# Kernel tuning notes

Measured on AMD Instinct MI355X. Metric: run time of the kernel, lower is better.

Reference implementation:

```python
import jax, jax.numpy as jnp
import numpy as np

S, B, D1, D2 = 256, 128, 1024, 1024
H1 = (D1 + D1) // 2  # 1024
H2 = (D1 + D2) // 2  # 1024


def setup_inputs() -> dict:
    key = jax.random.key(0)
    ks = jax.random.split(key, 11)
    s = lambda k, shp, fan_in: jax.random.normal(k, shp, jnp.float32) * (1.0 / np.sqrt(fan_in))
    return {
        "feature1": jax.random.normal(ks[0], (B, D1), jnp.float32),
        "feature2": jax.random.normal(ks[1], (B, D2), jnp.float32),
        "feature1_seq": jax.random.normal(ks[2], (S, B, D1), jnp.float32),
        "W11": s(ks[3], (2 * D1, H1), 2 * D1),
        "b11": jnp.zeros((H1,), jnp.float32),
        "W12": s(ks[4], (D1 + D2, H2), D1 + D2),
        "b12": jnp.zeros((H2,), jnp.float32),
        "W21": s(ks[5], (H1, 1), H1),
        "b21": jnp.zeros((1,), jnp.float32),
        "W22": s(ks[6], (H2, 1), H2),
        "b22": jnp.zeros((1,), jnp.float32),
    }


def reference(feature1, feature2, feature1_seq, W11, b11, W12, b12, W21, b21, W22, b22):
    # feature1_seq: [S, B, D1]; feature1: [B, D1]; feature2: [B, D2]
    seq_len = feature1_seq.shape[0]
    f1 = jnp.broadcast_to(feature1[None], (seq_len,) + feature1.shape)  # [S,B,D1]
    f2 = jnp.broadcast_to(feature2[None], (seq_len,) + feature2.shape)  # [S,B,D2]
    h1 = jnp.tanh(jnp.concatenate([feature1_seq, f1], axis=-1) @ W11 + b11)  # [S,B,H1]
    h2 = jnp.tanh(jnp.concatenate([feature1_seq, f2], axis=-1) @ W12 + b12)  # [S,B,H2]
    s1 = h1 @ W21 + b21  # [S,B,1]
    s2 = h2 @ W22 + b22  # [S,B,1]
    w1 = jax.nn.softmax(s1, axis=0)  # softmax over sequence dim
    w2 = jax.nn.softmax(s2, axis=0)
    # mean over sequence of (w1+w2)*seq/2 -> [B, D1]
    return jnp.mean((w1 + w2) * feature1_seq * 0.5, axis=0)
```

## Files before the change

### kernel.cpp

```cpp
#include <hip/hip_runtime.h>

#define S_LEN 256
#define B_SZ  128
#define M_ROWS (S_LEN * B_SZ)

typedef __attribute__((ext_vector_type(8))) short bf16x8;
typedef __attribute__((ext_vector_type(4))) float f32x4;

__device__ __forceinline__ unsigned short f2bf(float x) {
    unsigned u = __float_as_uint(x);
    unsigned r = (u + 0x7fffu + ((u >> 16) & 1u)) >> 16;
    return (unsigned short)r;
}

__device__ __forceinline__ void gl_lds16(const void* g, void* l) {
    __builtin_amdgcn_global_load_lds(
        (const __attribute__((address_space(1))) unsigned int*)g,
        (__attribute__((address_space(3))) unsigned int*)l,
        16, 0, 0);
}

__global__ __launch_bounds__(256) void convert_seq(const float* __restrict__ in,
                                                   unsigned short* __restrict__ out,
                                                   long n4) {
    long i = (long)blockIdx.x * blockDim.x + threadIdx.x;
    long stride = (long)gridDim.x * blockDim.x;
    for (; i < n4; i += stride) {
        float4 v = ((const float4*)in)[i];
        ushort4 o;
        o.x = f2bf(v.x); o.y = f2bf(v.y); o.z = f2bf(v.z); o.w = f2bf(v.w);
        ((ushort4*)out)[i] = o;
    }
}

__global__ __launch_bounds__(256) void convert_f(const float* __restrict__ f1,
                                                 const float* __restrict__ f2,
                                                 unsigned short* __restrict__ out) {
    int g = blockIdx.x * 256 + threadIdx.x;
    float4 v = (g < 32768) ? ((const float4*)f1)[g] : ((const float4*)f2)[g - 32768];
    ushort4 o;
    o.x = f2bf(v.x); o.y = f2bf(v.y); o.z = f2bf(v.z); o.w = f2bf(v.w);
    ((ushort4*)out)[g] = o;
}

__global__ __launch_bounds__(256) void transpose_w(const float* __restrict__ W11,
                                                   const float* __restrict__ W12,
                                                   unsigned short* __restrict__ Wt) {
    const int nt = blockIdx.x, kt = blockIdx.y, layer = blockIdx.z;
    const float* W = layer ? W12 : W11;
    __shared__ float T[64][65];
    const int c = threadIdx.x & 63, r4 = threadIdx.x >> 6;
    const int k0 = kt * 64, n0 = nt * 64;
    #pragma unroll
    for (int p = 0; p < 16; ++p) {
        int r = p * 4 + r4;
        T[r][c] = W[(size_t)(k0 + r) * 1024 + n0 + c];
    }
    __syncthreads();
    unsigned short* Wl = Wt + (size_t)layer * 1024 * 2048;
    #pragma unroll
    for (int p = 0; p < 16; ++p) {
        int n = p * 4 + r4;
        Wl[(size_t)(n0 + n) * 2048 + k0 + c] = f2bf(T[c][n]);
    }
}

__global__ __launch_bounds__(256) void c_precompute(const unsigned short* __restrict__ fbf,
                                                    const unsigned short* __restrict__ Wt,
                                                    const float* __restrict__ b11,
                                                    const float* __restrict__ b12,
                                                    float* __restrict__ cbuf) {
    __shared__ char smem[32768];
    unsigned short* ldsA = (unsigned short*)smem;
    unsigned short* ldsB = (unsigned short*)(smem + 16384);
    const int n0 = blockIdx.x * 128;
    const int layer = blockIdx.y;
    const int tid = threadIdx.x;
    const int w = tid >> 6, l = tid & 63;
    const int wm = w >> 1, wn = w & 1;
    const int lr = l & 15, lg = l >> 4;
    const unsigned short* Af = fbf + (size_t)layer * 128 * 1024;
    const unsigned short* Wl = Wt + (size_t)layer * 1024 * 2048;
    const float* bias = layer ? b12 : b11;

    f32x4 acc[4][4];
    #pragma unroll
    for (int i = 0; i < 4; ++i)
        #pragma unroll
        for (int j = 0; j < 4; ++j)
            #pragma unroll
            for (int e = 0; e < 4; ++e) acc[i][j][e] = 0.f;

    for (int kk = 0; kk < 1024; kk += 64) {
        __syncthreads();
        #pragma unroll
        for (int c = 0; c < 4; ++c) {
            int o = w * 4096 + c * 1024;
            int ob = o + l * 16;
            int row = ob >> 7, kb = ob & 127;
            gl_lds16((const char*)Af + ((size_t)row * 1024 + kk) * 2 + kb, (char*)ldsA + o);
            gl_lds16((const char*)Wl + ((size_t)(n0 + row) * 2048 + 1024 + kk) * 2 + kb, (char*)ldsB + o);
        }
        __syncthreads();
        #pragma unroll
        for (int ks = 0; ks < 2; ++ks) {
            bf16x8 av[4], bv[4];
            #pragma unroll
            for (int i = 0; i < 4; ++i) {
                av[i] = *(const bf16x8*)(ldsA + (wm * 64 + i * 16 + lr) * 64 + ks * 32 + lg * 8);
                bv[i] = *(const bf16x8*)(ldsB + (wn * 64 + i * 16 + lr) * 64 + ks * 32 + lg * 8);
            }
            #pragma unroll
            for (int i = 0; i < 4; ++i)
                #pragma unroll
                for (int j = 0; j < 4; ++j)
                    acc[i][j] = __builtin_amdgcn_mfma_f32_16x16x32_bf16(av[i], bv[j], acc[i][j], 0, 0, 0);
        }
    }
    float* cl = cbuf + (size_t)layer * 128 * 1024;
    #pragma unroll
    for (int i = 0; i < 4; ++i)
        #pragma unroll
        for (int j = 0; j < 4; ++j)
            #pragma unroll
            for (int q = 0; q < 4; ++q) {
                int rr = wm * 64 + i * 16 + lg * 4 + q;
                int hc = n0 + wn * 64 + j * 16 + lr;
                cl[(size_t)rr * 1024 + hc] = acc[i][j][q] + bias[hc];
            }
}


__global__ __launch_bounds__(1024, 4) void fused_main(const unsigned short* __restrict__ Abf,
                                                      const unsigned short* __restrict__ Wt,
                                                      const float* __restrict__ cbuf,
                                                      const float* __restrict__ W21,
                                                      const float* __restrict__ W22,
                                                      float* __restrict__ sbufp) {
    __shared__ char smem[65536];
    const int layer = blockIdx.x >> 2;
    const int nt    = blockIdx.x & 3;
    const int bx    = blockIdx.y;
    const int tid = threadIdx.x;
    const int w = tid >> 6, l = tid & 63;
    const int wm = w >> 2, wn = w & 3;
    const int lr = l & 15, lg = l >> 4;
    const int n0 = nt * 256;

    const char* Ag = (const char*)Abf + (size_t)bx * 256 * 2048;
    const char* Bg = (const char*)(Wt + (size_t)layer * 1024 * 2048) + (size_t)n0 * 4096;

    const int dloc = w * 1024 + l * 16;
    const int gsw  = dloc ^ (((dloc >> 7) & 3) << 4);
    const char* srcA = Ag + (size_t)(gsw >> 6) * 2048 + (gsw & 63);
    const char* srcB = Bg + (size_t)(gsw >> 6) * 4096 + (gsw & 63);

    f32x4 acc[4][4];
    #pragma unroll
    for (int i = 0; i < 4; ++i)
        #pragma unroll
        for (int j = 0; j < 4; ++j)
            #pragma unroll
            for (int e = 0; e < 4; ++e) acc[i][j][e] = 0.f;

    int offA[4], offB[4];
    #pragma unroll
    for (int i = 0; i < 4; ++i) {
        int oa = (wm * 64 + i * 16 + lr) * 64 + lg * 16;
        offA[i] = oa ^ (((oa >> 7) & 3) << 4);
        int ob = (wn * 64 + i * 16 + lr) * 64 + lg * 16;
        offB[i] = ob ^ (((ob >> 7) & 3) << 4);
    }

    gl_lds16(srcA, smem + w * 1024);
    gl_lds16(srcB, smem + 16384 + w * 1024);
    __syncthreads();

    for (int t = 0; t < 32; ++t) {
        const int cur = t & 1;
        if (t < 31) {
            char* db = smem + (cur ^ 1) * 32768 + w * 1024;
            gl_lds16(srcA + (size_t)(t + 1) * 64, db);
            gl_lds16(srcB + (size_t)(t + 1) * 64, db + 16384);
        }
        const char* Ab = smem + cur * 32768;
        const char* Bb = Ab + 16384;
        bf16x8 av[4], bv[4];
        #pragma unroll
        for (int i = 0; i < 4; ++i) av[i] = *(const bf16x8*)(Ab + offA[i]);
        #pragma unroll
        for (int j = 0; j < 4; ++j) bv[j] = *(const bf16x8*)(Bb + offB[j]);
        #pragma unroll
        for (int i = 0; i < 4; ++i)
            #pragma unroll
            for (int j = 0; j < 4; ++j)
                acc[i][j] = __builtin_amdgcn_mfma_f32_16x16x32_bf16(av[i], bv[j], acc[i][j], 0, 0, 0);
        __syncthreads();
    }

    const float* cl = cbuf + (size_t)layer * 131072;
    const float* W2 = layer ? W22 : W21;
    float w2v[4];
    #pragma unroll
    for (int j = 0; j < 4; ++j) w2v[j] = W2[n0 + wn * 64 + j * 16 + lr];
    float* red = (float*)smem;
    #pragma unroll
    for (int i = 0; i < 4; ++i) {
        #pragma unroll
        for (int q = 0; q < 4; ++q) {
            int wrow = wm * 64 + i * 16 + lg * 4 + q;
            int brow = wrow & 127;
            float p = 0.f;
            #pragma unroll
            for (int j = 0; j < 4; ++j) {
                int col = n0 + wn * 64 + j * 16 + lr;
                float z = acc[i][j][q] + cl[(size_t)brow * 1024 + col];
                float e = __expf(2.f * z);
                p += (1.f - 2.f / (e + 1.f)) * w2v[j];
            }
            p += __shfl_xor(p, 1);
            p += __shfl_xor(p, 2);
            p += __shfl_xor(p, 4);
            p += __shfl_xor(p, 8);
            if (lr == 0) red[wrow * 4 + wn] = p;
        }
    }
    __syncthreads();
    if (tid < 256) {
        float v = red[tid * 4 + 0] + red[tid * 4 + 1] + red[tid * 4 + 2] + red[tid * 4 + 3];
        sbufp[(size_t)blockIdx.x * M_ROWS + (size_t)bx * 256 + tid] = v;
    }
}

__device__ __forceinline__ float block_max(float v, float* lds) {
    #pragma unroll
    for (int m = 32; m; m >>= 1) v = fmaxf(v, __shfl_xor(v, m));
    if ((threadIdx.x & 63) == 0) lds[threadIdx.x >> 6] = v;
    __syncthreads();
    v = fmaxf(fmaxf(lds[0], lds[1]), fmaxf(lds[2], lds[3]));
    __syncthreads();
    return v;
}
__device__ __forceinline__ float block_sum(float v, float* lds) {
    #pragma unroll
    for (int m = 32; m; m >>= 1) v += __shfl_xor(v, m);
    if ((threadIdx.x & 63) == 0) lds[threadIdx.x >> 6] = v;
    __syncthreads();
    v = lds[0] + lds[1] + lds[2] + lds[3];
    __syncthreads();
    return v;
}

__global__ __launch_bounds__(256) void coef_kernel(const float* __restrict__ sbufp,
                                                   float* __restrict__ coef,
                                                   float* __restrict__ out) {
    __shared__ float lds[4];
    const int b = blockIdx.x, s = threadIdx.x;
    float v1 = 0.f, v2 = 0.f;
    #pragma unroll
    for (int nt = 0; nt < 4; ++nt) {
        v1 += sbufp[(size_t)nt * M_ROWS + (size_t)s * 128 + b];
        v2 += sbufp[(size_t)(4 + nt) * M_ROWS + (size_t)s * 128 + b];
    }
    float m1 = block_max(v1, lds);
    float e1 = expf(v1 - m1);
    float S1 = block_sum(e1, lds);
    float m2 = block_max(v2, lds);
    float e2 = expf(v2 - m2);
    float S2 = block_sum(e2, lds);
    coef[(size_t)s * 128 + b] = (e1 / S1 + e2 / S2) * (0.5f / (float)S_LEN);
    float4 z4; z4.x = z4.y = z4.z = z4.w = 0.f;
    ((float4*)out)[(size_t)b * 256 + s] = z4;
}

__global__ __launch_bounds__(256) void final_kernel(const float* __restrict__ seq,
                                                    const float* __restrict__ coef,
                                                    float* __restrict__ out) {
    const int b = blockIdx.x, q = blockIdx.y;
    const int d0 = threadIdx.x * 4;
    float4 a; a.x = a.y = a.z = a.w = 0.f;
    for (int si = 0; si < 32; ++si) {
        int s = q * 32 + si;
        float cf = coef[(size_t)s * 128 + b];
        float4 v = *(const float4*)(seq + ((size_t)(s * 128 + b) * 1024 + d0));
        a.x += cf * v.x; a.y += cf * v.y; a.z += cf * v.z; a.w += cf * v.w;
    }
    float* o = out + (size_t)b * 1024 + d0;
    atomicAdd(o + 0, a.x);
    atomicAdd(o + 1, a.y);
    atomicAdd(o + 2, a.z);
    atomicAdd(o + 3, a.w);
}

extern "C" void kernel_launch(void* const* d_in, const int* in_sizes, int n_in,
                              void* d_out, int out_size, void* d_ws, size_t ws_size,
                              hipStream_t stream) {
    const float* feature1 = (const float*)d_in[0];
    const float* feature2 = (const float*)d_in[1];
    const float* seq      = (const float*)d_in[2];
    const float* W11      = (const float*)d_in[3];
    const float* b11      = (const float*)d_in[4];
    const float* W12      = (const float*)d_in[5];
    const float* b12      = (const float*)d_in[6];
    const float* W21      = (const float*)d_in[7];
    const float* W22      = (const float*)d_in[9];
    float* out = (float*)d_out;

    char* ws = (char*)d_ws;
    unsigned short* Abf   = (unsigned short*)(ws + 0);
    unsigned short* Wt    = (unsigned short*)(ws + 67108864);
    unsigned short* fbf   = (unsigned short*)(ws + 75497472);
    float*          cbuf  = (float*)(ws + 76021760);
    float*          sbufp = (float*)(ws + 77070336);
    float*          coef  = (float*)(ws + 78118912);

    convert_seq<<<2048, 256, 0, stream>>>(seq, Abf, (long)M_ROWS * 1024 / 4);
    convert_f<<<256, 256, 0, stream>>>(feature1, feature2, fbf);
    transpose_w<<<dim3(16, 32, 2), 256, 0, stream>>>(W11, W12, Wt);
    c_precompute<<<dim3(8, 2), 256, 0, stream>>>(fbf, Wt, b11, b12, cbuf);
    fused_main<<<dim3(8, 128), 1024, 0, stream>>>(Abf, Wt, cbuf, W21, W22, sbufp);
    coef_kernel<<<128, 256, 0, stream>>>(sbufp, coef, out);
    final_kernel<<<dim3(128, 8), 256, 0, stream>>>(seq, coef, out);
}
```

Before: 258.7 us.

## Triple-buffer GEMM loads with 512-thread blocks and remapped tile order

The main fused GEMM kernel moves from 1024 threads with 4x4 MFMA tiles per wave to 512 threads with 8x4 tiles per wave, so each wave gets more register-level reuse of its B fragments. The double-buffered LDS pipeline becomes a three-stage pipeline with explicit vmcnt waits and raw barriers, keeping two loads in flight during compute. Block indices are remapped so consecutive blocks share the same weight tile and nearby A rows, to improve cache locality. The cost is more accumulator registers and more LDS (96 KB), which lowers occupancy.

```diff
diff --git a/kernel.cpp b/kernel.cpp
--- a/kernel.cpp
+++ b/kernel.cpp
@@ -131,72 +131,114 @@
 }
 
 
-__global__ __launch_bounds__(1024, 4) void fused_main(const unsigned short* __restrict__ Abf,
-                                                      const unsigned short* __restrict__ Wt,
-                                                      const float* __restrict__ cbuf,
-                                                      const float* __restrict__ W21,
-                                                      const float* __restrict__ W22,
-                                                      float* __restrict__ sbufp) {
-    __shared__ char smem[65536];
-    const int layer = blockIdx.x >> 2;
-    const int nt    = blockIdx.x & 3;
-    const int bx    = blockIdx.y;
+__global__ __launch_bounds__(512, 2) void fused_main(const unsigned short* __restrict__ Abf,
+                                                     const unsigned short* __restrict__ Wt,
+                                                     const float* __restrict__ cbuf,
+                                                     const float* __restrict__ W21,
+                                                     const float* __restrict__ W22,
+                                                     float* __restrict__ sbufp) {
+    __shared__ char smem[98304];
+    const int bid = blockIdx.x;
+    const int r8  = bid & 7;
+    const int jj  = bid >> 3;
+    const int mt  = r8 + 8 * (jj & 15);
+    const int g   = jj >> 4;
+    const int layer = g >> 2;
+    const int nt    = g & 3;
+    const int n0 = nt * 256;
+
     const int tid = threadIdx.x;
     const int w = tid >> 6, l = tid & 63;
     const int wm = w >> 2, wn = w & 3;
     const int lr = l & 15, lg = l >> 4;
-    const int n0 = nt * 256;
-
-    const char* Ag = (const char*)Abf + (size_t)bx * 256 * 2048;
+
+    const char* Ag = (const char*)Abf + (size_t)mt * 256 * 2048;
     const char* Bg = (const char*)(Wt + (size_t)layer * 1024 * 2048) + (size_t)n0 * 4096;
 
-    const int dloc = w * 1024 + l * 16;
-    const int gsw  = dloc ^ (((dloc >> 7) & 3) << 4);
-    const char* srcA = Ag + (size_t)(gsw >> 6) * 2048 + (gsw & 63);
-    const char* srcB = Bg + (size_t)(gsw >> 6) * 4096 + (gsw & 63);
-
-    f32x4 acc[4][4];
-    #pragma unroll
-    for (int i = 0; i < 4; ++i)
+    const int dl0 = w * 1024 + l * 16;
+    const int dl1 = 8192 + dl0;
+    const int g0 = dl0 ^ (((dl0 >> 7) & 3) << 4);
+    const int g1 = dl1 ^ (((dl1 >> 7) & 3) << 4);
+    const char* srcA0 = Ag + (size_t)(g0 >> 6) * 2048 + (g0 & 63);
+    const char* srcA1 = Ag + (size_t)(g1 >> 6) * 2048 + (g1 & 63);
+    const char* srcB0 = Bg + (size_t)(g0 >> 6) * 4096 + (g0 & 63);
+    const char* srcB1 = Bg + (size_t)(g1 >> 6) * 4096 + (g1 & 63);
+    const int dstA0 = w * 1024, dstA1 = 8192 + w * 1024;
+
+    f32x4 acc[8][4];
+    #pragma unroll
+    for (int i = 0; i < 8; ++i)
         #pragma unroll
         for (int j = 0; j < 4; ++j)
             #pragma unroll
             for (int e = 0; e < 4; ++e) acc[i][j][e] = 0.f;
 
-    int offA[4], offB[4];
-    #pragma unroll
-    for (int i = 0; i < 4; ++i) {
-        int oa = (wm * 64 + i * 16 + lr) * 64 + lg * 16;
+    int offA[8], offB[4];
+    #pragma unroll
+    for (int i = 0; i < 8; ++i) {
+        int oa = (wm * 128 + i * 16 + lr) * 64 + lg * 16;
         offA[i] = oa ^ (((oa >> 7) & 3) << 4);
-        int ob = (wn * 64 + i * 16 + lr) * 64 + lg * 16;
-        offB[i] = ob ^ (((ob >> 7) & 3) << 4);
-    }
-
-    gl_lds16(srcA, smem + w * 1024);
-    gl_lds16(srcB, smem + 16384 + w * 1024);
-    __syncthreads();
-
-    for (int t = 0; t < 32; ++t) {
-        const int cur = t & 1;
-        if (t < 31) {
-            char* db = smem + (cur ^ 1) * 32768 + w * 1024;
-            gl_lds16(srcA + (size_t)(t + 1) * 64, db);
-            gl_lds16(srcB + (size_t)(t + 1) * 64, db + 16384);
-        }
-        const char* Ab = smem + cur * 32768;
-        const char* Bb = Ab + 16384;
-        bf16x8 av[4], bv[4];
-        #pragma unroll
-        for (int i = 0; i < 4; ++i) av[i] = *(const bf16x8*)(Ab + offA[i]);
-        #pragma unroll
-        for (int j = 0; j < 4; ++j) bv[j] = *(const bf16x8*)(Bb + offB[j]);
-        #pragma unroll
-        for (int i = 0; i < 4; ++i)
-            #pragma unroll
-            for (int j = 0; j < 4; ++j)
-                acc[i][j] = __builtin_amdgcn_mfma_f32_16x16x32_bf16(av[i], bv[j], acc[i][j], 0, 0, 0);
-        __syncthreads();
-    }
+    }
+    #pragma unroll
+    for (int j = 0; j < 4; ++j) {
+        int ob = (wn * 64 + j * 16 + lr) * 64 + lg * 16;
+        offB[j] = ob ^ (((ob >> 7) & 3) << 4);
+    }
+
+#define STAGE(t, bi) do {                                              \
+        char* ab_ = smem + (bi) * 32768;                               \
+        gl_lds16(srcA0 + (size_t)(t) * 64, ab_ + dstA0);               \
+        gl_lds16(srcA1 + (size_t)(t) * 64, ab_ + dstA1);               \
+        gl_lds16(srcB0 + (size_t)(t) * 64, ab_ + 16384 + dstA0);       \
+        gl_lds16(srcB1 + (size_t)(t) * 64, ab_ + 16384 + dstA1);       \
+    } while (0)
+
+#define COMPUTE(bi) do {                                               \
+        const char* Ab_ = smem + (bi) * 32768;                         \
+        const char* Bb_ = Ab_ + 16384;                                 \
+        bf16x8 av_[8], bv_[4];                                         \
+        _Pragma("unroll")                                              \
+        for (int i_ = 0; i_ < 8; ++i_) av_[i_] = *(const bf16x8*)(Ab_ + offA[i_]); \
+        _Pragma("unroll")                                              \
+        for (int j_ = 0; j_ < 4; ++j_) bv_[j_] = *(const bf16x8*)(Bb_ + offB[j_]); \
+        _Pragma("unroll")                                              \
+        for (int i_ = 0; i_ < 8; ++i_)                                 \
+            _Pragma("unroll")                                          \
+            for (int j_ = 0; j_ < 4; ++j_)                             \
+                acc[i_][j_] = __builtin_amdgcn_mfma_f32_16x16x32_bf16( \
+                    av_[i_], bv_[j_], acc[i_][j_], 0, 0, 0);           \
+    } while (0)
+
+#define PIPEBAR() do {                                                 \
+        __builtin_amdgcn_sched_barrier(0);                             \
+        asm volatile("s_waitcnt vmcnt(4)" ::: "memory");               \
+        __builtin_amdgcn_sched_barrier(0);                             \
+        __builtin_amdgcn_s_barrier();                                  \
+        __builtin_amdgcn_sched_barrier(0);                             \
+    } while (0)
+
+    STAGE(0, 0);
+    STAGE(1, 1);
+    PIPEBAR();
+
+    for (int tt = 0; tt < 30; tt += 3) {
+        STAGE(tt + 2, 2); COMPUTE(0); PIPEBAR();
+        STAGE(tt + 3, 0); COMPUTE(1); PIPEBAR();
+        STAGE(tt + 4, 1); COMPUTE(2); PIPEBAR();
+    }
+    COMPUTE(0);
+    __builtin_amdgcn_sched_barrier(0);
+    asm volatile("s_waitcnt vmcnt(0)" ::: "memory");
+    __builtin_amdgcn_sched_barrier(0);
+    __builtin_amdgcn_s_barrier();
+    __builtin_amdgcn_sched_barrier(0);
+    COMPUTE(1);
+
+#undef STAGE
+#undef COMPUTE
+#undef PIPEBAR
+
+    __syncthreads();
 
     const float* cl = cbuf + (size_t)layer * 131072;
     const float* W2 = layer ? W22 : W21;
@@ -205,10 +247,10 @@
     for (int j = 0; j < 4; ++j) w2v[j] = W2[n0 + wn * 64 + j * 16 + lr];
     float* red = (float*)smem;
     #pragma unroll
-    for (int i = 0; i < 4; ++i) {
+    for (int i = 0; i < 8; ++i) {
         #pragma unroll
         for (int q = 0; q < 4; ++q) {
-            int wrow = wm * 64 + i * 16 + lg * 4 + q;
+            int wrow = wm * 128 + i * 16 + lg * 4 + q;
             int brow = wrow & 127;
             float p = 0.f;
             #pragma unroll
@@ -228,7 +270,7 @@
     __syncthreads();
     if (tid < 256) {
         float v = red[tid * 4 + 0] + red[tid * 4 + 1] + red[tid * 4 + 2] + red[tid * 4 + 3];
-        sbufp[(size_t)blockIdx.x * M_ROWS + (size_t)bx * 256 + tid] = v;
+        sbufp[(size_t)g * M_ROWS + (size_t)mt * 256 + tid] = v;
     }
 }
 
@@ -318,7 +360,7 @@
     convert_f<<<256, 256, 0, stream>>>(feature1, feature2, fbf);
     transpose_w<<<dim3(16, 32, 2), 256, 0, stream>>>(W11, W12, Wt);
     c_precompute<<<dim3(8, 2), 256, 0, stream>>>(fbf, Wt, b11, b12, cbuf);
-    fused_main<<<dim3(8, 128), 1024, 0, stream>>>(Abf, Wt, cbuf, W21, W22, sbufp);
+    fused_main<<<1024, 512, 0, stream>>>(Abf, Wt, cbuf, W21, W22, sbufp);
     coef_kernel<<<128, 256, 0, stream>>>(sbufp, coef, out);
     final_kernel<<<dim3(128, 8), 256, 0, stream>>>(seq, coef, out);
 }
```

Measured after the change: 276.2 us. +6.8%, slower.
